# Kernel optimization log

Hardware: AMD Instinct MI355X
Metric: run time of the kernel (lower is better)

## Reference

```python
import jax, jax.numpy as jnp
import numpy as np

N_NODES = 100000
N_EDGES = 1600000
DIM_IN, DIM_H, DIM_OUT = 64, 64, 16


def setup_inputs() -> dict:
    key = jax.random.key(0)
    ks = jax.random.split(key, 7)
    s = lambda d: 1.0 / np.sqrt(d)
    return {
        "x": jax.random.normal(ks[0], (N_NODES, DIM_IN), dtype=jnp.float32),
        "edge_index": jax.random.randint(ks[1], (2, N_EDGES), 0, N_NODES, dtype=jnp.int32),
        "W1l": jax.random.normal(ks[2], (DIM_IN, DIM_H), dtype=jnp.float32) * s(DIM_IN),
        "W1r": jax.random.normal(ks[3], (DIM_IN, DIM_H), dtype=jnp.float32) * s(DIM_IN),
        "b1": jnp.zeros((DIM_H,), dtype=jnp.float32),
        "W2l": jax.random.normal(ks[4], (DIM_H, DIM_OUT), dtype=jnp.float32) * s(DIM_H),
        "W2r": jax.random.normal(ks[5], (DIM_H, DIM_OUT), dtype=jnp.float32) * s(DIM_H),
        "b2": jnp.zeros((DIM_OUT,), dtype=jnp.float32),
    }


def _sage_conv(h, edge_index, Wl, Wr, b):
    # PyG SAGEConv (mean aggr): out = mean_{j in N(i)} h_j @ Wl + h_i @ Wr + b
    src, dst = edge_index[0], edge_index[1]
    n = h.shape[0]
    agg = jax.ops.segment_sum(h[src], dst, num_segments=n)          # [N, d]
    deg = jax.ops.segment_sum(jnp.ones_like(dst, dtype=h.dtype), dst, num_segments=n)
    mean = agg / jnp.maximum(deg, 1.0)[:, None]
    return mean @ Wl + h @ Wr + b


def reference(x, edge_index, W1l, W1r, b1, W2l, W2r, b2):
    h = jax.nn.relu(_sage_conv(x, edge_index, W1l, W1r, b1))
    # dropout(p=0.5) is identity in eval mode (training=False)
    h = _sage_conv(h, edge_index, W2l, W2r, b2)
    return jax.nn.log_softmax(h, axis=1)
```

## Files before the change

### kernel.cpp

```cpp
#include <hip/hip_runtime.h>
#include <cstdint>
#include <cstddef>


typedef float f32x4 __attribute__((ext_vector_type(4)));
typedef float f32x2 __attribute__((ext_vector_type(2)));
typedef short short8 __attribute__((ext_vector_type(8)));
typedef __bf16 bf16x8 __attribute__((ext_vector_type(8)));

#define BK 256
#define NBMAX 512
#define CAP 5120
#define TILE 8192
#define WCAP 512

__device__ __forceinline__ unsigned f2bf(float f) {
    unsigned u = __float_as_uint(f);
    u += 0x7FFFu + ((u >> 16) & 1u);
    return u >> 16;
}

__device__ __forceinline__ f32x4 mfma16(short8 a, short8 b, f32x4 c) {
    return __builtin_amdgcn_mfma_f32_16x16x32_bf16(
        __builtin_bit_cast(bf16x8, a), __builtin_bit_cast(bf16x8, b), c, 0, 0, 0);
}

__device__ __forceinline__ void glds16(const void* g, void* l) {
    __builtin_amdgcn_global_load_lds(
        (const __attribute__((address_space(1))) unsigned int*)g,
        (__attribute__((address_space(3))) unsigned int*)l, 16, 0, 0);
}

#define ACC2(r, alo, ahi)                     \
    alo += __uint_as_float((r) << 16);        \
    ahi += __uint_as_float(r);

#define ACCF8(w, i)                                                   \
    {                                                                 \
        f32x2 f0 = __builtin_amdgcn_cvt_pk_f32_fp8((w), false);       \
        f32x2 f1 = __builtin_amdgcn_cvt_pk_f32_fp8((w), true);        \
        acc[(i)] += f0.x; acc[(i) + 1] += f0.y;                       \
        acc[(i) + 2] += f1.x; acc[(i) + 3] += f1.y;                   \
    }
#define ACCQ(v)                                                       \
    { ACCF8((v).x, 0); ACCF8((v).y, 4); ACCF8((v).z, 8); ACCF8((v).w, 12); }

__global__ __launch_bounds__(512) void partprep_k(
    const int* __restrict__ ei, int* __restrict__ bcnt,
    unsigned* __restrict__ part, int E, int pblocks,
    const float* __restrict__ x, unsigned short* __restrict__ xb,
    unsigned char* __restrict__ xq, int n,
    const float* __restrict__ W1l, const float* __restrict__ W1r,
    const float* __restrict__ W2l, const float* __restrict__ W2r,
    unsigned short* __restrict__ bimg, int xblocks) {
    __shared__ int scn[NBMAX], sbase[NBMAX], lofs[NBMAX], cur[NBMAX];
    __shared__ unsigned stageW[TILE];
    __shared__ unsigned short stageB[TILE];
    int t = threadIdx.x;
    int bid = blockIdx.x;

    if (bid >= pblocks) {
        int cb = bid - pblocks;
        if (cb < xblocks) {
            int i = (cb * 512 + t) * 8;
            if (i >= n) return;
            const float4* xp = (const float4*)(x + i);
            float4 a = xp[0], b = xp[1];
            uint4 o;
            o.x = f2bf(a.x) | (f2bf(a.y) << 16);
            o.y = f2bf(a.z) | (f2bf(a.w) << 16);
            o.z = f2bf(b.x) | (f2bf(b.y) << 16);
            o.w = f2bf(b.z) | (f2bf(b.w) << 16);
            *(uint4*)(xb + i) = o;
            int w0 = __builtin_amdgcn_cvt_pk_fp8_f32(a.x, a.y, 0, false);
            w0 = __builtin_amdgcn_cvt_pk_fp8_f32(a.z, a.w, w0, true);
            int w1 = __builtin_amdgcn_cvt_pk_fp8_f32(b.x, b.y, 0, false);
            w1 = __builtin_amdgcn_cvt_pk_fp8_f32(b.z, b.w, w1, true);
            *(uint2*)(xq + i) = make_uint2((unsigned)w0, (unsigned)w1);
            return;
        }
        int e = (cb - xblocks) * 512 + t;
        if (e >= 20 * 64) return;
        int f = e >> 6, L = e & 63;
        int qd = L >> 4, m = L & 15;
        unsigned o[8];
        if (f < 16) {
            int kb = f >> 2, nb = f & 3;
            int n2 = nb * 16 + m;
#pragma unroll
            for (int j = 0; j < 8; ++j) {
                int k = kb * 32 + qd * 8 + j;
                float v = (k < 64) ? W1l[k * 64 + n2] : W1r[(k - 64) * 64 + n2];
                o[j] = f2bf(v);
            }
        } else {
            int g = f - 16;
            int kb = g >> 1, nb = g & 1;
#pragma unroll
            for (int j = 0; j < 8; ++j) {
                int k = kb * 32 + qd * 8 + j;
                float v = nb ? W2r[k * 16 + m] : W2l[k * 16 + m];
                o[j] = f2bf(v);
            }
        }
        uint4 pk;
        pk.x = o[0] | (o[1] << 16);
        pk.y = o[2] | (o[3] << 16);
        pk.z = o[4] | (o[5] << 16);
        pk.w = o[6] | (o[7] << 16);
        ((uint4*)bimg)[e] = pk;
        return;
    }

    int base = bid * TILE;
    cur[t] = 0;
    __syncthreads();
    int4 s4[4], d4[4];
#pragma unroll
    for (int i = 0; i < 4; ++i) {
        int e0 = base + (t + i * 512) * 4;
        if (e0 < E) {
            s4[i] = ((const int4*)ei)[e0 >> 2];
            d4[i] = ((const int4*)(ei + E))[e0 >> 2];
        } else {
            d4[i] = make_int4(-1, -1, -1, -1);
            s4[i] = make_int4(0, 0, 0, 0);
        }
    }
    int rk[16];
#pragma unroll
    for (int i = 0; i < 4; ++i) {
        int d[4] = {d4[i].x, d4[i].y, d4[i].z, d4[i].w};
#pragma unroll
        for (int u = 0; u < 4; ++u)
            rk[i * 4 + u] = (d[u] >= 0) ? atomicAdd(&cur[d[u] >> 8], 1) : 0;
    }
    __syncthreads();
    int own = cur[t];
    scn[t] = own;
    __syncthreads();
    for (int off = 1; off < NBMAX; off <<= 1) {
        int v = (t >= off) ? scn[t - off] : 0;
        __syncthreads();
        scn[t] += v;
        __syncthreads();
    }
    lofs[t] = scn[t] - own;
    if (own > 0) sbase[t] = atomicAdd(&bcnt[t], own);
    __syncthreads();
#pragma unroll
    for (int i = 0; i < 4; ++i) {
        int s[4] = {s4[i].x, s4[i].y, s4[i].z, s4[i].w};
        int d[4] = {d4[i].x, d4[i].y, d4[i].z, d4[i].w};
#pragma unroll
        for (int u = 0; u < 4; ++u) {
            if (d[u] < 0) continue;
            int b = d[u] >> 8;
            int pos = lofs[b] + rk[i * 4 + u];
            stageW[pos] = ((unsigned)(d[u] & (BK - 1)) << 17) | (unsigned)s[u];
            stageB[pos] = (unsigned short)b;
        }
    }
    __syncthreads();
    int tot = scn[NBMAX - 1];
    for (int q = t; q < tot; q += 512) {
        int b = stageB[q];
        part[b * CAP + sbase[b] + (q - lofs[b])] = stageW[q];
    }
}

__global__ __launch_bounds__(256) void csr_k(const unsigned* __restrict__ part,
                                             const int* __restrict__ bcnt,
                                             int* __restrict__ csr,
                                             int2* __restrict__ rowse, int N) {
    __shared__ int h[BK];
    __shared__ int s[BK];
    int b = blockIdx.x, t = threadIdx.x;
    int cnt = bcnt[b];
    int base = b * CAP;
    h[t] = 0;
    __syncthreads();
    for (int q = t; q < cnt; q += 256)
        atomicAdd(&h[(part[base + q] >> 17) & (BK - 1)], 1);
    __syncthreads();
    int own = h[t];
    s[t] = own;
    __syncthreads();
    for (int off = 1; off < BK; off <<= 1) {
        int v = (t >= off) ? s[t - off] : 0;
        __syncthreads();
        s[t] += v;
        __syncthreads();
    }
    int excl = s[t] - own;
    int node = b * BK + t;
    if (node < N) rowse[node] = make_int2(base + excl, base + excl + own);
    __syncthreads();
    h[t] = excl;
    __syncthreads();
    for (int q = t; q < cnt; q += 256) {
        unsigned w = part[base + q];
        int pos = atomicAdd(&h[(w >> 17) & (BK - 1)], 1);
        csr[base + pos] = (int)(w & 0x1FFFFu);
    }
}

__global__ __launch_bounds__(256, 6) void l1x(
    const unsigned short* __restrict__ xb, const unsigned char* __restrict__ xq,
    const int2* __restrict__ rowse, const int* __restrict__ csr,
    const unsigned short* __restrict__ bimg,
    const float* __restrict__ b1, const float* __restrict__ b2,
    unsigned short* __restrict__ p, float* __restrict__ q, int N) {
    __shared__ __align__(16) unsigned char sbuf[4][4096];
    __shared__ int wcsr[4][WCAP];
    int t = threadIdx.x;
    int wave = t >> 6, lane = t & 63;
    int nodebase = blockIdx.x * 64 + wave * 16;
    int grp = lane >> 2, sub = lane & 3;
    int node = nodebase + grp;
    int2 be = (node < N) ? rowse[node] : make_int2(0, 0);

    int qd = lane >> 4, m = lane & 15;
    int mynode = nodebase + m;
    short8 afr2 = {0, 0, 0, 0, 0, 0, 0, 0};
    short8 afr3 = {0, 0, 0, 0, 0, 0, 0, 0};
    if (mynode < N) {
        afr2 = *(const short8*)(xb + ((size_t)mynode << 6) + qd * 8);
        afr3 = *(const short8*)(xb + ((size_t)mynode << 6) + 32 + qd * 8);
    }

    int wstart = 0, wlen = 0;
    if (nodebase < N) {
        int ln = min(nodebase + 15, N - 1);
        wstart = rowse[nodebase].x;
        wlen = rowse[ln].y - wstart;
    }
    bool useLds = (wlen <= WCAP);
    if (useLds) {
        for (int i = lane; i < wlen; i += 64) wcsr[wave][i] = csr[wstart + i];
    }

    float acc[16];
#pragma unroll
    for (int i = 0; i < 16; ++i) acc[i] = 0.f;
    if (useLds) {
        const int* wc = &wcsr[wave][0];
        unsigned char* stg = &sbuf[wave][0];
        int k = be.x - wstart, kend = be.y - wstart;
        while (__any(k < kend)) {
#pragma unroll
            for (int j = 0; j < 4; ++j) {
                if (k + j < kend) {
                    int src = wc[k + j];
                    glds16(xq + ((size_t)src << 6) + (sub << 4),
                           stg + j * 1024);
                }
            }
            asm volatile("s_waitcnt vmcnt(0)" ::: "memory");
#pragma unroll
            for (int j = 0; j < 4; ++j) {
                if (k + j < kend) {
                    uint4 a = *(const uint4*)(stg + j * 1024 + (lane << 4));
                    ACCQ(a);
                }
            }
            k += 4;
        }
    } else {
        int k = be.x, kend = be.y;
        for (; k + 1 < kend; k += 2) {
            int s0 = csr[k], s1 = csr[k + 1];
            uint4 a = ((const uint4*)(xq + ((size_t)s0 << 6)))[sub];
            uint4 b = ((const uint4*)(xq + ((size_t)s1 << 6)))[sub];
            ACCQ(a); ACCQ(b);
        }
        if (k < kend) {
            int s0 = csr[k];
            uint4 a = ((const uint4*)(xq + ((size_t)s0 << 6)))[sub];
            ACCQ(a);
        }
    }
    unsigned short (*mh)[72] = (unsigned short (*)[72])&sbuf[wave][0];
    {
        float rd = 1.0f / fmaxf((float)(be.y - be.x), 1.0f);
        uint4 o0, o1;
        o0.x = f2bf(acc[0] * rd) | (f2bf(acc[1] * rd) << 16);
        o0.y = f2bf(acc[2] * rd) | (f2bf(acc[3] * rd) << 16);
        o0.z = f2bf(acc[4] * rd) | (f2bf(acc[5] * rd) << 16);
        o0.w = f2bf(acc[6] * rd) | (f2bf(acc[7] * rd) << 16);
        o1.x = f2bf(acc[8] * rd) | (f2bf(acc[9] * rd) << 16);
        o1.y = f2bf(acc[10] * rd) | (f2bf(acc[11] * rd) << 16);
        o1.z = f2bf(acc[12] * rd) | (f2bf(acc[13] * rd) << 16);
        o1.w = f2bf(acc[14] * rd) | (f2bf(acc[15] * rd) << 16);
        *(uint4*)&mh[grp][sub * 16] = o0;
        *(uint4*)&mh[grp][sub * 16 + 8] = o1;
    }

    const short8* bfr = (const short8*)bimg;
    short8 afr0 = *(const short8*)&mh[m][qd * 8];
    short8 afr1 = *(const short8*)&mh[m][32 + qd * 8];

#pragma unroll
    for (int nb = 0; nb < 4; ++nb) {
        f32x4 c = {0.f, 0.f, 0.f, 0.f};
        c = mfma16(afr0, bfr[nb * 64 + lane], c);
        c = mfma16(afr1, bfr[(4 + nb) * 64 + lane], c);
        c = mfma16(afr2, bfr[(8 + nb) * 64 + lane], c);
        c = mfma16(afr3, bfr[(12 + nb) * 64 + lane], c);
        int col = nb * 16 + m;
        float bb = b1[col];
#pragma unroll
        for (int r = 0; r < 4; ++r) {
            float hv = fmaxf(c[r] + bb, 0.0f);
            mh[qd * 4 + r][col] = (unsigned short)f2bf(hv);
        }
    }

    short8 ha0 = *(const short8*)&mh[m][qd * 8];
    short8 ha1 = *(const short8*)&mh[m][32 + qd * 8];
    f32x4 pc = {0.f, 0.f, 0.f, 0.f}, qc = {0.f, 0.f, 0.f, 0.f};
    pc = mfma16(ha0, bfr[16 * 64 + lane], pc);
    pc = mfma16(ha1, bfr[18 * 64 + lane], pc);
    qc = mfma16(ha0, bfr[17 * 64 + lane], qc);
    qc = mfma16(ha1, bfr[19 * 64 + lane], qc);
    float b2v = b2[m];
#pragma unroll
    for (int r = 0; r < 4; ++r) {
        int nd = nodebase + qd * 4 + r;
        if (nd < N) {
            p[(size_t)nd * 16 + m] = (unsigned short)f2bf(pc[r]);
            q[(size_t)nd * 16 + m] = qc[r] + b2v;
        }
    }
}

__global__ __launch_bounds__(256) void finalk(const unsigned short* __restrict__ p,
                                              const int2* __restrict__ rowse,
                                              const int* __restrict__ csr,
                                              float* q, int N) {
    __shared__ int wcsr[4][WCAP];
    int t = threadIdx.x;
    int wave = t >> 6, lane = t & 63;
    int grp = lane >> 2, sub = lane & 3;
    int nodebase = blockIdx.x * 64 + wave * 16;
    int node = nodebase + grp;
    int2 be = (node < N) ? rowse[node] : make_int2(0, 0);

    int wstart = 0, wlen = 0;
    if (nodebase < N) {
        int ln = min(nodebase + 15, N - 1);
        wstart = rowse[nodebase].x;
        wlen = rowse[ln].y - wstart;
    }
    bool useLds = (wlen <= WCAP);
    if (useLds) {
        for (int i = lane; i < wlen; i += 64) wcsr[wave][i] = csr[wstart + i];
    }
    if (node >= N) return;

    float4 qv = ((const float4*)(q + ((size_t)node << 4)))[sub];
    float a0 = 0.f, a1 = 0.f, a2 = 0.f, a3 = 0.f;
    if (useLds) {
        const int* wc = &wcsr[wave][0];
        int k = be.x - wstart, kend = be.y - wstart;
        for (; k + 1 < kend; k += 2) {
            uint2 rA = *(const uint2*)(p + ((size_t)wc[k] << 4) + (sub << 2));
            uint2 rB = *(const uint2*)(p + ((size_t)wc[k + 1] << 4) + (sub << 2));
            ACC2(rA.x, a0, a1);  ACC2(rA.y, a2, a3);
            ACC2(rB.x, a0, a1);  ACC2(rB.y, a2, a3);
        }
        if (k < kend) {
            uint2 rA = *(const uint2*)(p + ((size_t)wc[k] << 4) + (sub << 2));
            ACC2(rA.x, a0, a1);  ACC2(rA.y, a2, a3);
        }
    } else {
        int k = be.x, kend = be.y;
        for (; k + 1 < kend; k += 2) {
            int s0 = csr[k], s1 = csr[k + 1];
            uint2 rA = *(const uint2*)(p + ((size_t)s0 << 4) + (sub << 2));
            uint2 rB = *(const uint2*)(p + ((size_t)s1 << 4) + (sub << 2));
            ACC2(rA.x, a0, a1);  ACC2(rA.y, a2, a3);
            ACC2(rB.x, a0, a1);  ACC2(rB.y, a2, a3);
        }
        if (k < kend) {
            int s0 = csr[k];
            uint2 rA = *(const uint2*)(p + ((size_t)s0 << 4) + (sub << 2));
            ACC2(rA.x, a0, a1);  ACC2(rA.y, a2, a3);
        }
    }
    float rd = 1.0f / fmaxf((float)(be.y - be.x), 1.0f);
    float4 v = {a0 * rd + qv.x, a1 * rd + qv.y, a2 * rd + qv.z, a3 * rd + qv.w};
    float mm = fmaxf(fmaxf(v.x, v.y), fmaxf(v.z, v.w));
    mm = fmaxf(mm, __shfl_xor(mm, 1));
    mm = fmaxf(mm, __shfl_xor(mm, 2));
    float s = __expf(v.x - mm) + __expf(v.y - mm) + __expf(v.z - mm) + __expf(v.w - mm);
    s += __shfl_xor(s, 1);
    s += __shfl_xor(s, 2);
    float ls = __logf(s);
    float4 o = {v.x - mm - ls, v.y - mm - ls, v.z - mm - ls, v.w - mm - ls};
    ((float4*)(q + ((size_t)node << 4)))[sub] = o;
}

extern "C" void kernel_launch(void* const* d_in, const int* in_sizes, int n_in,
                              void* d_out, int out_size, void* d_ws, size_t ws_size,
                              hipStream_t stream) {
    const float* x   = (const float*)d_in[0];
    const int* ei    = (const int*)d_in[1];
    const float* W1l = (const float*)d_in[2];
    const float* W1r = (const float*)d_in[3];
    const float* b1  = (const float*)d_in[4];
    const float* W2l = (const float*)d_in[5];
    const float* W2r = (const float*)d_in[6];
    const float* b2  = (const float*)d_in[7];
    const int N = in_sizes[0] / 64;
    const int E = in_sizes[1] / 2;
    const int nbk = (N + BK - 1) / BK;

    int*  bcnt  = (int*)d_ws;
    int2* rowse = (int2*)(bcnt + NBMAX);
    int*  csr   = (int*)(rowse + N);
    unsigned short* bimg = (unsigned short*)(csr + (size_t)nbk * CAP);
    unsigned short* p    = bimg + 20 * 64 * 8;
    unsigned* part = (unsigned*)(p + (size_t)N * 16);
    unsigned short* xb = (unsigned short*)(part + (size_t)nbk * CAP);
    unsigned char* xq = (unsigned char*)(xb + (size_t)N * 64);
    float* q = (float*)d_out;

    hipMemsetAsync(bcnt, 0, NBMAX * sizeof(int), stream);

    const int pblocks = (E + TILE - 1) / TILE;
    const int xblocks = (N * 64 + 4095) / 4096;
    partprep_k<<<pblocks + xblocks + 3, 512, 0, stream>>>(
        ei, bcnt, part, E, pblocks, x, xb, xq, N * 64, W1l, W1r, W2l, W2r,
        bimg, xblocks);
    csr_k<<<nbk, 256, 0, stream>>>(part, bcnt, csr, rowse, N);
    l1x<<<(N + 63) / 64, 256, 0, stream>>>(xb, xq, rowse, csr, bimg, b1, b2,
                                           p, q, N);
    finalk<<<(N + 63) / 64, 256, 0, stream>>>(p, rowse, csr, q, N);
}
```

Baseline: 156.9 us.

## Split FP8 feature table into two half-width arrays and gather in two passes

Stores the FP8 node features as two separate 32-byte-per-node arrays (features 0-31 and 32-63) and runs the layer-1 neighbor gather as two passes, one per half. Each gather pass touches a smaller 3.2MB table that fits cache better, and each lane handles two edges per load slot with 8 accumulators instead of 16, which lowers register pressure. In exchange the CSR neighbor lists are walked twice, the loop overhead and load instructions double, and each gathered row becomes a 32-byte access, so DRAM sector efficiency may drop.

```diff
diff --git a/kernel.cpp b/kernel.cpp
--- a/kernel.cpp
+++ b/kernel.cpp
@@ -42,14 +42,12 @@
         acc[(i)] += f0.x; acc[(i) + 1] += f0.y;                       \
         acc[(i) + 2] += f1.x; acc[(i) + 3] += f1.y;                   \
     }
-#define ACCQ(v)                                                       \
-    { ACCF8((v).x, 0); ACCF8((v).y, 4); ACCF8((v).z, 8); ACCF8((v).w, 12); }
 
 __global__ __launch_bounds__(512) void partprep_k(
     const int* __restrict__ ei, int* __restrict__ bcnt,
     unsigned* __restrict__ part, int E, int pblocks,
     const float* __restrict__ x, unsigned short* __restrict__ xb,
-    unsigned char* __restrict__ xq, int n,
+    unsigned char* __restrict__ xqA, unsigned char* __restrict__ xqB, int n,
     const float* __restrict__ W1l, const float* __restrict__ W1r,
     const float* __restrict__ W2l, const float* __restrict__ W2r,
     unsigned short* __restrict__ bimg, int xblocks) {
@@ -76,7 +74,10 @@
             w0 = __builtin_amdgcn_cvt_pk_fp8_f32(a.z, a.w, w0, true);
             int w1 = __builtin_amdgcn_cvt_pk_fp8_f32(b.x, b.y, 0, false);
             w1 = __builtin_amdgcn_cvt_pk_fp8_f32(b.z, b.w, w1, true);
-            *(uint2*)(xq + i) = make_uint2((unsigned)w0, (unsigned)w1);
+            int node = i >> 6, feat = i & 63;
+            unsigned char* dst = (feat < 32) ? (xqA + (size_t)node * 32 + feat)
+                                             : (xqB + (size_t)node * 32 + (feat - 32));
+            *(uint2*)dst = make_uint2((unsigned)w0, (unsigned)w1);
             return;
         }
         int e = (cb - xblocks) * 512 + t;
@@ -206,7 +207,8 @@
 }
 
 __global__ __launch_bounds__(256, 6) void l1x(
-    const unsigned short* __restrict__ xb, const unsigned char* __restrict__ xq,
+    const unsigned short* __restrict__ xb,
+    const unsigned char* __restrict__ xqA, const unsigned char* __restrict__ xqB,
     const int2* __restrict__ rowse, const int* __restrict__ csr,
     const unsigned short* __restrict__ bimg,
     const float* __restrict__ b1, const float* __restrict__ b2,
@@ -240,61 +242,99 @@
         for (int i = lane; i < wlen; i += 64) wcsr[wave][i] = csr[wstart + i];
     }
 
-    float acc[16];
-#pragma unroll
-    for (int i = 0; i < 16; ++i) acc[i] = 0.f;
+    const int* wc = &wcsr[wave][0];
+    unsigned char* stg = &sbuf[wave][0];
+    int kbeg = be.x - wstart, kend = be.y - wstart;
+    int pairsel = sub >> 1;
+    int half = sub & 1;
+    int rbase = ((lane >> 2) << 6);
+    float rd = 1.0f / fmaxf((float)(be.y - be.x), 1.0f);
+    float acc[8];
+    uint4 oA, oB;
+
+#pragma unroll
+    for (int i = 0; i < 8; ++i) acc[i] = 0.f;
     if (useLds) {
-        const int* wc = &wcsr[wave][0];
-        unsigned char* stg = &sbuf[wave][0];
-        int k = be.x - wstart, kend = be.y - wstart;
+        int k = kbeg;
         while (__any(k < kend)) {
 #pragma unroll
             for (int j = 0; j < 4; ++j) {
-                if (k + j < kend) {
-                    int src = wc[k + j];
-                    glds16(xq + ((size_t)src << 6) + (sub << 4),
+                int e = k + 2 * j + pairsel;
+                if (e < kend) {
+                    int src = wc[e];
+                    glds16(xqA + ((size_t)src << 5) + (half << 4),
                            stg + j * 1024);
                 }
             }
             asm volatile("s_waitcnt vmcnt(0)" ::: "memory");
 #pragma unroll
             for (int j = 0; j < 4; ++j) {
-                if (k + j < kend) {
-                    uint4 a = *(const uint4*)(stg + j * 1024 + (lane << 4));
-                    ACCQ(a);
-                }
-            }
-            k += 4;
+                if (k + 2 * j < kend) {
+                    uint2 r = *(const uint2*)(stg + j * 1024 + rbase + sub * 8);
+                    ACCF8(r.x, 0); ACCF8(r.y, 4);
+                }
+                if (k + 2 * j + 1 < kend) {
+                    uint2 r = *(const uint2*)(stg + j * 1024 + rbase + 32 + sub * 8);
+                    ACCF8(r.x, 0); ACCF8(r.y, 4);
+                }
+            }
+            k += 8;
         }
     } else {
-        int k = be.x, kend = be.y;
-        for (; k + 1 < kend; k += 2) {
-            int s0 = csr[k], s1 = csr[k + 1];
-            uint4 a = ((const uint4*)(xq + ((size_t)s0 << 6)))[sub];
-            uint4 b = ((const uint4*)(xq + ((size_t)s1 << 6)))[sub];
-            ACCQ(a); ACCQ(b);
-        }
-        if (k < kend) {
+        for (int k = be.x; k < be.y; ++k) {
             int s0 = csr[k];
-            uint4 a = ((const uint4*)(xq + ((size_t)s0 << 6)))[sub];
-            ACCQ(a);
-        }
-    }
-    unsigned short (*mh)[72] = (unsigned short (*)[72])&sbuf[wave][0];
-    {
-        float rd = 1.0f / fmaxf((float)(be.y - be.x), 1.0f);
-        uint4 o0, o1;
-        o0.x = f2bf(acc[0] * rd) | (f2bf(acc[1] * rd) << 16);
-        o0.y = f2bf(acc[2] * rd) | (f2bf(acc[3] * rd) << 16);
-        o0.z = f2bf(acc[4] * rd) | (f2bf(acc[5] * rd) << 16);
-        o0.w = f2bf(acc[6] * rd) | (f2bf(acc[7] * rd) << 16);
-        o1.x = f2bf(acc[8] * rd) | (f2bf(acc[9] * rd) << 16);
-        o1.y = f2bf(acc[10] * rd) | (f2bf(acc[11] * rd) << 16);
-        o1.z = f2bf(acc[12] * rd) | (f2bf(acc[13] * rd) << 16);
-        o1.w = f2bf(acc[14] * rd) | (f2bf(acc[15] * rd) << 16);
-        *(uint4*)&mh[grp][sub * 16] = o0;
-        *(uint4*)&mh[grp][sub * 16 + 8] = o1;
-    }
+            uint2 r = *(const uint2*)(xqA + ((size_t)s0 << 5) + (sub << 3));
+            ACCF8(r.x, 0); ACCF8(r.y, 4);
+        }
+    }
+    oA.x = f2bf(acc[0] * rd) | (f2bf(acc[1] * rd) << 16);
+    oA.y = f2bf(acc[2] * rd) | (f2bf(acc[3] * rd) << 16);
+    oA.z = f2bf(acc[4] * rd) | (f2bf(acc[5] * rd) << 16);
+    oA.w = f2bf(acc[6] * rd) | (f2bf(acc[7] * rd) << 16);
+
+#pragma unroll
+    for (int i = 0; i < 8; ++i) acc[i] = 0.f;
+    if (useLds) {
+        int k = kbeg;
+        while (__any(k < kend)) {
+#pragma unroll
+            for (int j = 0; j < 4; ++j) {
+                int e = k + 2 * j + pairsel;
+                if (e < kend) {
+                    int src = wc[e];
+                    glds16(xqB + ((size_t)src << 5) + (half << 4),
+                           stg + j * 1024);
+                }
+            }
+            asm volatile("s_waitcnt vmcnt(0)" ::: "memory");
+#pragma unroll
+            for (int j = 0; j < 4; ++j) {
+                if (k + 2 * j < kend) {
+                    uint2 r = *(const uint2*)(stg + j * 1024 + rbase + sub * 8);
+                    ACCF8(r.x, 0); ACCF8(r.y, 4);
+                }
+                if (k + 2 * j + 1 < kend) {
+                    uint2 r = *(const uint2*)(stg + j * 1024 + rbase + 32 + sub * 8);
+                    ACCF8(r.x, 0); ACCF8(r.y, 4);
+                }
+            }
+            k += 8;
+        }
+    } else {
+        for (int k = be.x; k < be.y; ++k) {
+            int s0 = csr[k];
+            uint2 r = *(const uint2*)(xqB + ((size_t)s0 << 5) + (sub << 3));
+            ACCF8(r.x, 0); ACCF8(r.y, 4);
+        }
+    }
+    oB.x = f2bf(acc[0] * rd) | (f2bf(acc[1] * rd) << 16);
+    oB.y = f2bf(acc[2] * rd) | (f2bf(acc[3] * rd) << 16);
+    oB.z = f2bf(acc[4] * rd) | (f2bf(acc[5] * rd) << 16);
+    oB.w = f2bf(acc[6] * rd) | (f2bf(acc[7] * rd) << 16);
+
+    unsigned short (*mh)[72] = (unsigned short (*)[72])stg;
+    *(uint4*)&mh[grp][sub * 8] = oA;
+    *(uint4*)&mh[grp][32 + sub * 8] = oB;
 
     const short8* bfr = (const short8*)bimg;
     short8 afr0 = *(const short8*)&mh[m][qd * 8];
@@ -423,7 +463,8 @@
     unsigned short* p    = bimg + 20 * 64 * 8;
     unsigned* part = (unsigned*)(p + (size_t)N * 16);
     unsigned short* xb = (unsigned short*)(part + (size_t)nbk * CAP);
-    unsigned char* xq = (unsigned char*)(xb + (size_t)N * 64);
+    unsigned char* xqA = (unsigned char*)(xb + (size_t)N * 64);
+    unsigned char* xqB = xqA + (size_t)N * 32;
     float* q = (float*)d_out;
 
     hipMemsetAsync(bcnt, 0, NBMAX * sizeof(int), stream);
@@ -431,10 +472,10 @@
     const int pblocks = (E + TILE - 1) / TILE;
     const int xblocks = (N * 64 + 4095) / 4096;
     partprep_k<<<pblocks + xblocks + 3, 512, 0, stream>>>(
-        ei, bcnt, part, E, pblocks, x, xb, xq, N * 64, W1l, W1r, W2l, W2r,
-        bimg, xblocks);
+        ei, bcnt, part, E, pblocks, x, xb, xqA, xqB, N * 64, W1l, W1r, W2l,
+        W2r, bimg, xblocks);
     csr_k<<<nbk, 256, 0, stream>>>(part, bcnt, csr, rowse, N);
-    l1x<<<(N + 63) / 64, 256, 0, stream>>>(xb, xq, rowse, csr, bimg, b1, b2,
-                                           p, q, N);
+    l1x<<<(N + 63) / 64, 256, 0, stream>>>(xb, xqA, xqB, rowse, csr, bimg,
+                                           b1, b2, p, q, N);
     finalk<<<(N + 63) / 64, 256, 0, stream>>>(p, rowse, csr, q, N);
 }
```

After: 163.4 us. 4.1% more time.
